# Performance work log

Hardware: AMD Instinct MI355X
Metric: run time of the kernel (lower is better)

The kernel has to match this reference:

```python
import jax, jax.numpy as jnp
import numpy as np

B, L, H, D = 2, 2048, 16, 64
E = H * D  # 1024

def setup_inputs() -> dict:
    key = jax.random.key(0)
    k1, k2, k3 = jax.random.split(key, 3)
    net_in = jax.random.normal(k1, (B, L, E), dtype=jnp.float32)
    # torch nn.Linear weights are [out_features, in_features]; scale like kaiming-uniform-ish
    W_qkv = jax.random.normal(k2, (3 * E, E), dtype=jnp.float32) * (1.0 / np.sqrt(E))
    W_out = jax.random.normal(k3, (E, E), dtype=jnp.float32) * (1.0 / np.sqrt(E))
    return {"net_in": net_in, "W_qkv": W_qkv, "W_out": W_out}

def reference(net_in, W_qkv, W_out):
    b, l, c = net_in.shape
    h, d = H, D
    # c_proj: x @ W_qkv.T -> (B, L, 3E), split into q, k, v
    qkv = jnp.einsum('blc,ec->ble', net_in, W_qkv)
    q, k, v = jnp.split(qkv, 3, axis=-1)
    # reshape to (B, H, L, D)
    q = q.reshape(b, l, h, d).transpose(0, 2, 1, 3)
    k = k.reshape(b, l, h, d).transpose(0, 2, 1, 3)
    v = v.reshape(b, l, h, d).transpose(0, 2, 1, 3)
    scale = 1.0 / np.sqrt(d).astype(np.float32)
    attn = jnp.einsum('bhqd,bhkd->bhqk', q, k) * scale  # (B, H, L, L)
    causal = jnp.tril(jnp.ones((l, l), dtype=bool))
    attn = jnp.where(causal[None, None, :, :], attn, -jnp.inf)
    attn = jax.nn.softmax(attn, axis=-1)
    out = jnp.einsum('bhqk,bhkd->bhqd', attn, v)  # (B, H, L, D)
    out = out.transpose(0, 2, 1, 3).reshape(b, l, c)
    return jnp.einsum('blc,ec->ble', out, W_out)
```

## Files before the change

kernel.cpp:

```cpp
#include <hip/hip_runtime.h>
#include <hip/hip_bf16.h>

#define LOG2E 1.44269504088896340736f

typedef __attribute__((ext_vector_type(8))) short s16x8;
typedef __attribute__((ext_vector_type(4))) short s16x4;
typedef __attribute__((ext_vector_type(2))) unsigned int u32x2;
typedef __attribute__((ext_vector_type(4))) float f32x4;
typedef __attribute__((ext_vector_type(16))) float f32x16;

__device__ inline short f2bf(float f) {
  __hip_bfloat16 h = __float2bfloat16(f);
  union { __hip_bfloat16 h; short s; } u; u.h = h; return u.s;
}

__device__ inline unsigned cvtpk(float lo, float hi) {
  unsigned r;
  asm("v_cvt_pk_bf16_f32 %0, %1, %2" : "=v"(r) : "v"(lo), "v"(hi));
  return r;
}

__device__ inline void gl_lds16(const void* g, void* l) {
  __builtin_amdgcn_global_load_lds(
      (const __attribute__((address_space(1))) void*)g,
      (__attribute__((address_space(3))) void*)l, 16, 0, 0);
}

__global__ __launch_bounds__(256)
void cvt_all(const float* __restrict__ Wqkv, const float* __restrict__ Wout,
             const float* __restrict__ net,
             short* __restrict__ dWqkv, short* __restrict__ dWout,
             short* __restrict__ dnet) {
  int bid = blockIdx.x;
  const float* src; short* dst; int i;
  if (bid < 3072)      { src = Wqkv; dst = dWqkv; i = bid * 256 + threadIdx.x; }
  else if (bid < 4096) { src = Wout; dst = dWout; i = (bid - 3072) * 256 + threadIdx.x; }
  else                 { src = net;  dst = dnet;  i = (bid - 4096) * 256 + threadIdx.x; }
  f32x4 v = ((const f32x4*)src)[i];
  s16x4 o;
  o[0] = f2bf(v[0]); o[1] = f2bf(v[1]); o[2] = f2bf(v[2]); o[3] = f2bf(v[3]);
  ((s16x4*)dst)[i] = o;
}

template<int OUTF32, int VTRANS, int NSUB>
__global__ __launch_bounds__(256)
void gemm128(const short* __restrict__ A, int lda,
             const short* __restrict__ B, int ldb,
             void* __restrict__ Cp, int ldc, int K) {
  int id = (int)(blockIdx.x + (blockIdx.y << 5));
  int xcd = id & 7, slot = id >> 3;
  int m0 = (slot & 31) * 128;
  int n0 = (xcd * NSUB + (slot >> 5)) * 128;
  int t = threadIdx.x;
  int w = t >> 6, lane = t & 63;
  int l16 = lane & 15, quad = lane >> 4;
  int wm = w >> 1, wn = w & 1;

  __shared__ __align__(16) short As[2][128 * 32];
  __shared__ __align__(16) short Bs[2][128 * 32];

  int scell = ((t & 3) ^ ((t >> 3) & 3)) * 8;
  const short* bsrc = B + (size_t)(n0 + (t >> 2)) * ldb + scell;
  const short* asrc = A + (size_t)(m0 + (t >> 2)) * lda + scell;
  int rcell = (quad ^ ((l16 >> 1) & 3)) * 8;

  f32x4 acc[4][4];
#pragma unroll
  for (int i = 0; i < 4; ++i)
#pragma unroll
    for (int j = 0; j < 4; ++j) acc[i][j] = (f32x4){0.f, 0.f, 0.f, 0.f};

#pragma unroll
  for (int r = 0; r < 2; ++r) {
    gl_lds16(asrc + (size_t)r * 64 * lda, (char*)As + r * 4096 + w * 1024);
    gl_lds16(bsrc + (size_t)r * 64 * ldb, (char*)Bs + r * 4096 + w * 1024);
  }
  __syncthreads();

  int nks = K >> 5;
  for (int ks = 0; ks < nks; ++ks) {
    int cur = ks & 1;
    if (ks + 1 < nks) {
      int k0 = (ks + 1) * 32;
      int nb = cur ^ 1;
#pragma unroll
      for (int r = 0; r < 2; ++r) {
        gl_lds16(asrc + k0 + (size_t)r * 64 * lda, (char*)As + nb * 8192 + r * 4096 + w * 1024);
        gl_lds16(bsrc + k0 + (size_t)r * 64 * ldb, (char*)Bs + nb * 8192 + r * 4096 + w * 1024);
      }
    }

    s16x8 af[4], bf[4];
#pragma unroll
    for (int i = 0; i < 4; ++i) {
      af[i] = *(const s16x8*)(As[cur] + (wm * 64 + i * 16 + l16) * 32 + rcell);
      bf[i] = *(const s16x8*)(Bs[cur] + (wn * 64 + i * 16 + l16) * 32 + rcell);
    }
#pragma unroll
    for (int i = 0; i < 4; ++i)
#pragma unroll
      for (int j = 0; j < 4; ++j)
        acc[i][j] = __builtin_amdgcn_mfma_f32_16x16x32_bf16(af[i], bf[j], acc[i][j], 0, 0, 0);

    __syncthreads();
  }

  if (VTRANS && n0 >= 2048) {
    short* Cs = (short*)Cp;
#pragma unroll
    for (int i = 0; i < 4; ++i)
#pragma unroll
      for (int j = 0; j < 4; ++j) {
        int colg = n0 + wn * 64 + j * 16 + l16;
        int d = colg & 63;
        size_t dst = (size_t)(m0 + wm * 64 + d) * ldc + (colg - d) + i * 16 + quad * 4;
        s16x4 ob;
#pragma unroll
        for (int rr = 0; rr < 4; ++rr) ob[rr] = f2bf(acc[i][j][rr]);
        *(s16x4*)(Cs + dst) = ob;
      }
  } else {
#pragma unroll
    for (int i = 0; i < 4; ++i)
#pragma unroll
      for (int j = 0; j < 4; ++j)
#pragma unroll
        for (int rr = 0; rr < 4; ++rr) {
          size_t row = m0 + wm * 64 + i * 16 + quad * 4 + rr;
          size_t col = n0 + wn * 64 + j * 16 + l16;
          if (OUTF32) ((float*)Cp)[row * ldc + col] = acc[i][j][rr];
          else        ((short*)Cp)[row * ldc + col] = f2bf(acc[i][j][rr]);
        }
  }
}

__global__ __launch_bounds__(256)
void gemm64(const short* __restrict__ A, int lda,
            const short* __restrict__ B, int ldb,
            float* __restrict__ C, int ldc, int K) {
  int id = (int)(blockIdx.x + (blockIdx.y << 5));
  int xcd = id & 7, slot = id >> 3;
  int m0 = slot * 64;
  int n0 = xcd * 128;
  int t = threadIdx.x;
  int w = t >> 6, lane = t & 63;
  int l16 = lane & 15, quad = lane >> 4;
  int wm = w & 1, wn = w >> 1;

  __shared__ __align__(16) short As[2][64 * 32];
  __shared__ __align__(16) short Bs[2][128 * 32];

  int scell = ((t & 3) ^ ((t >> 3) & 3)) * 8;
  const short* asrc = A + (size_t)(m0 + (t >> 2)) * lda + scell;
  const short* bsrc = B + (size_t)(n0 + (t >> 2)) * ldb + scell;
  int rcell = (quad ^ ((l16 >> 1) & 3)) * 8;

  f32x4 acc[2][4];
#pragma unroll
  for (int i = 0; i < 2; ++i)
#pragma unroll
    for (int j = 0; j < 4; ++j) acc[i][j] = (f32x4){0.f, 0.f, 0.f, 0.f};

  gl_lds16(asrc, (char*)As + w * 1024);
#pragma unroll
  for (int r = 0; r < 2; ++r)
    gl_lds16(bsrc + (size_t)r * 64 * ldb, (char*)Bs + r * 4096 + w * 1024);
  __syncthreads();

  int nks = K >> 5;
  for (int ks = 0; ks < nks; ++ks) {
    int cur = ks & 1;
    if (ks + 1 < nks) {
      int k0 = (ks + 1) * 32;
      int nb = cur ^ 1;
      gl_lds16(asrc + k0, (char*)As + nb * 4096 + w * 1024);
#pragma unroll
      for (int r = 0; r < 2; ++r)
        gl_lds16(bsrc + k0 + (size_t)r * 64 * ldb, (char*)Bs + nb * 8192 + r * 4096 + w * 1024);
    }

    s16x8 af[2], bf[4];
#pragma unroll
    for (int i = 0; i < 2; ++i)
      af[i] = *(const s16x8*)(As[cur] + (wm * 32 + i * 16 + l16) * 32 + rcell);
#pragma unroll
    for (int j = 0; j < 4; ++j)
      bf[j] = *(const s16x8*)(Bs[cur] + (wn * 64 + j * 16 + l16) * 32 + rcell);
#pragma unroll
    for (int i = 0; i < 2; ++i)
#pragma unroll
      for (int j = 0; j < 4; ++j)
        acc[i][j] = __builtin_amdgcn_mfma_f32_16x16x32_bf16(af[i], bf[j], acc[i][j], 0, 0, 0);

    __syncthreads();
  }

#pragma unroll
  for (int i = 0; i < 2; ++i)
#pragma unroll
    for (int j = 0; j < 4; ++j)
#pragma unroll
      for (int rr = 0; rr < 4; ++rr) {
        size_t row = m0 + wm * 32 + i * 16 + quad * 4 + rr;
        size_t col = n0 + wn * 64 + j * 16 + l16;
        C[row * ldc + col] = acc[i][j][rr];
      }
}

__global__ __launch_bounds__(256, 4)
void attn(short* __restrict__ qkv) {
  const int L = 2048, E3 = 3072, EO = 1024;
  int id = (int)(blockIdx.x + (blockIdx.y << 5));
  int xcd = id & 7;
  int s = id >> 3;
  int bh = xcd * 4 + (s & 3);
  int u = s >> 2;
  int vv = u & 15;
  int qidx = (u & 16) ? (31 - vv) : vv;
  int b = bh >> 4, h = bh & 15;
  int q0 = qidx * 64;
  int t = threadIdx.x;
  int wave = t >> 6, lane = t & 63;
  int qh = wave >> 1, kh = wave & 1;
  int l31 = lane & 31, hsel = lane >> 5;
  int khi4 = hsel * 4;
  int key = (lane >> 1) & 3;
  const float SENT = -3.0e38f;
  const float SC = 0.125f * LOG2E;

  __shared__ __align__(16) short Ks[2][2][64][32];
  __shared__ __align__(16) short Vt[2][2][64][32];

  int rowbase = b * L;

  s16x8 qf[4];
  {
    const short* qp = qkv + (size_t)(rowbase + q0 + qh * 32 + l31) * E3 + h * 64 + hsel * 8;
#pragma unroll
    for (int e = 0; e < 4; ++e) {
      s16x8 raw = *(const s16x8*)(qp + e * 16);
#pragma unroll
      for (int j = 0; j < 8; ++j) {
        union { float f; int i; } u2; u2.i = ((int)(unsigned short)raw[j]) << 16;
        raw[j] = f2bf(u2.f * SC);
      }
      qf[e] = raw;
    }
  }

  int scell = ((lane & 3) ^ ((lane >> 3) & 3)) * 8;
  const short* ksrc = qkv + (size_t)(rowbase + wave * 16 + (lane >> 2)) * E3 + EO
                      + h * 64 + scell;
  const short* vsrc = qkv + (size_t)(rowbase + wave * 16 + (lane >> 2)) * E3 + 2 * EO
                      + h * 64 + scell;

  float l_acc = 0.f;
  f32x16 o0 = (f32x16){0.f,0.f,0.f,0.f,0.f,0.f,0.f,0.f,0.f,0.f,0.f,0.f,0.f,0.f,0.f,0.f};
  f32x16 o1 = o0;

  int nkb = qidx + 1;

  gl_lds16(ksrc,      (char*)Ks + wave * 1024);
  gl_lds16(ksrc + 32, (char*)Ks + 4096 + wave * 1024);
  gl_lds16(vsrc,      (char*)Vt + wave * 1024);
  gl_lds16(vsrc + 32, (char*)Vt + 4096 + wave * 1024);

  for (int kb = 0; kb < nkb; ++kb) {
    int cur = kb & 1;
    __syncthreads();
    if (kb + 1 < nkb) {
      size_t koff = (size_t)((kb + 1) * 64) * E3;
      int nb = cur ^ 1;
      gl_lds16(ksrc + koff,      (char*)Ks + nb * 8192 + wave * 1024);
      gl_lds16(ksrc + koff + 32, (char*)Ks + nb * 8192 + 4096 + wave * 1024);
      gl_lds16(vsrc + koff,      (char*)Vt + nb * 8192 + wave * 1024);
      gl_lds16(vsrc + koff + 32, (char*)Vt + nb * 8192 + 4096 + wave * 1024);
    }

    int rel = (q0 + qh * 32) - (kb * 64 + kh * 32);
    if (rel > -32) {
      int krow = kh * 32 + l31;
      s16x8 kf0 = *(const s16x8*)(&Ks[cur][0][krow][((0 + hsel) ^ key) * 8]);
      s16x8 kf1 = *(const s16x8*)(&Ks[cur][0][krow][((2 + hsel) ^ key) * 8]);
      s16x8 kf2 = *(const s16x8*)(&Ks[cur][1][krow][((0 + hsel) ^ key) * 8]);
      s16x8 kf3 = *(const s16x8*)(&Ks[cur][1][krow][((2 + hsel) ^ key) * 8]);
      s16x8 vf00 = *(const s16x8*)(&Vt[cur][kh][ 0 + l31][((0 + hsel) ^ key) * 8]);
      s16x8 vf01 = *(const s16x8*)(&Vt[cur][kh][32 + l31][((0 + hsel) ^ key) * 8]);
      s16x8 vf10 = *(const s16x8*)(&Vt[cur][kh][ 0 + l31][((2 + hsel) ^ key) * 8]);
      s16x8 vf11 = *(const s16x8*)(&Vt[cur][kh][32 + l31][((2 + hsel) ^ key) * 8]);

      f32x16 sf = (f32x16){0.f,0.f,0.f,0.f,0.f,0.f,0.f,0.f,0.f,0.f,0.f,0.f,0.f,0.f,0.f,0.f};
      sf = __builtin_amdgcn_mfma_f32_32x32x16_bf16(kf0, qf[0], sf, 0, 0, 0);
      sf = __builtin_amdgcn_mfma_f32_32x32x16_bf16(kf1, qf[1], sf, 0, 0, 0);
      sf = __builtin_amdgcn_mfma_f32_32x32x16_bf16(kf2, qf[2], sf, 0, 0, 0);
      sf = __builtin_amdgcn_mfma_f32_32x32x16_bf16(kf3, qf[3], sf, 0, 0, 0);

      if (rel < 31) {
        int thr = rel + l31 - khi4;
#pragma unroll
        for (int r = 0; r < 16; ++r) {
          const int base_k = (r & 3) + 8 * (r >> 2);
          if (base_k > thr) sf[r] = SENT;
        }
      }

      float pv[16];
#pragma unroll
      for (int r = 0; r < 16; ++r) {
        pv[r] = __builtin_amdgcn_exp2f(sf[r]);
        l_acc += pv[r];
      }

      unsigned A0 = cvtpk(pv[0],  pv[1]),  A1 = cvtpk(pv[2],  pv[3]);
      unsigned B0 = cvtpk(pv[4],  pv[5]),  B1 = cvtpk(pv[6],  pv[7]);
      unsigned C0 = cvtpk(pv[8],  pv[9]),  C1 = cvtpk(pv[10], pv[11]);
      unsigned D0 = cvtpk(pv[12], pv[13]), D1 = cvtpk(pv[14], pv[15]);
      u32x2 sw0 = __builtin_amdgcn_permlane32_swap(A0, B0, false, false);
      u32x2 sw1 = __builtin_amdgcn_permlane32_swap(A1, B1, false, false);
      u32x2 sw2 = __builtin_amdgcn_permlane32_swap(C0, D0, false, false);
      u32x2 sw3 = __builtin_amdgcn_permlane32_swap(C1, D1, false, false);
      union { s16x8 v; unsigned u[4]; } P0, P1;
      P0.u[0] = sw0[0]; P0.u[1] = sw1[0]; P0.u[2] = sw0[1]; P0.u[3] = sw1[1];
      P1.u[0] = sw2[0]; P1.u[1] = sw3[0]; P1.u[2] = sw2[1]; P1.u[3] = sw3[1];

      o0 = __builtin_amdgcn_mfma_f32_32x32x16_bf16(vf00, P0.v, o0, 0, 0, 0);
      o0 = __builtin_amdgcn_mfma_f32_32x32x16_bf16(vf10, P1.v, o0, 0, 0, 0);
      o1 = __builtin_amdgcn_mfma_f32_32x32x16_bf16(vf01, P0.v, o1, 0, 0, 0);
      o1 = __builtin_amdgcn_mfma_f32_32x32x16_bf16(vf11, P1.v, o1, 0, 0, 0);
    }
  }

  l_acc += __shfl_xor(l_acc, 32);
  __syncthreads();
  float* fs = (float*)&Ks[0][0][0][0];
  float* lb = (float*)&Vt[0][0][0][0];
  if (kh) {
#pragma unroll
    for (int r = 0; r < 16; ++r) {
      fs[qh * 2048 + r * 64 + lane] = o0[r];
      fs[qh * 2048 + (16 + r) * 64 + lane] = o1[r];
    }
    if (lane < 32) lb[qh * 32 + lane] = l_acc;
  }
  __syncthreads();
  if (!kh) {
    float inv = 1.f / (l_acc + lb[qh * 32 + l31]);
    size_t obase = (size_t)(rowbase + q0 + qh * 32 + l31) * E3 + h * 64;
    int fb = qh * 2048;
#pragma unroll
    for (int g = 0; g < 4; ++g) {
      s16x4 w0, w1;
#pragma unroll
      for (int rr = 0; rr < 4; ++rr) {
        int r = g * 4 + rr;
        w0[rr] = f2bf((o0[r] + fs[fb + r * 64 + lane]) * inv);
        w1[rr] = f2bf((o1[r] + fs[fb + (16 + r) * 64 + lane]) * inv);
      }
      *(s16x4*)(qkv + obase + g * 8 + khi4) = w0;
      *(s16x4*)(qkv + obase + 32 + g * 8 + khi4) = w1;
    }
  }
}

extern "C" void kernel_launch(void* const* d_in, const int* in_sizes, int n_in,
                              void* d_out, int out_size, void* d_ws, size_t ws_size,
                              hipStream_t stream) {
  const float* net_in = (const float*)d_in[0];
  const float* W_qkv  = (const float*)d_in[1];
  const float* W_out  = (const float*)d_in[2];

  short* Wqkvb = (short*)d_ws;
  short* Woutb = Wqkvb + (size_t)3072 * 1024;
  short* qkv   = Woutb + (size_t)1024 * 1024;
  short* netb  = (short*)d_out;

  cvt_all<<<8192, 256, 0, stream>>>(W_qkv, W_out, net_in, Wqkvb, Woutb, netb);

  gemm128<0, 1, 3><<<dim3(32, 24), 256, 0, stream>>>(netb, 1024, Wqkvb, 1024,
                                                     qkv, 3072, 1024);
  attn<<<dim3(32, 32), 256, 0, stream>>>(qkv);
  gemm64<<<dim3(32, 16), 256, 0, stream>>>(qkv, 3072, Woutb, 1024,
                                           (float*)d_out, 1024, 1024);
}
```

Before: 165.0 us.

## Replace QKV projection GEMM with 256x256 tile, 8-wave, deeply pipelined kernel

Swaps the 128x128, 4-wave QKV GEMM for a 256x256 tile kernel with 512 threads. It uses 64-wide K steps, a 128KB double-buffered LDS ring with XOR swizzle, and interleaves global-to-LDS loads with MFMA phases using explicit barriers, vmcnt waits and setprio. The larger tile raises arithmetic intensity and cuts redundant operand loads, and the interleaving hides memory latency. In exchange only 192 blocks launch, which is under one block per CU on 256 CUs, and the kernel hardcodes the problem dimensions.

```diff
diff --git a/kernel.cpp b/kernel.cpp
--- a/kernel.cpp
+++ b/kernel.cpp
@@ -42,94 +42,134 @@
   ((s16x4*)dst)[i] = o;
 }
 
-template<int OUTF32, int VTRANS, int NSUB>
-__global__ __launch_bounds__(256)
-void gemm128(const short* __restrict__ A, int lda,
-             const short* __restrict__ B, int ldb,
-             void* __restrict__ Cp, int ldc, int K) {
-  int id = (int)(blockIdx.x + (blockIdx.y << 5));
-  int xcd = id & 7, slot = id >> 3;
-  int m0 = (slot & 31) * 128;
-  int n0 = (xcd * NSUB + (slot >> 5)) * 128;
+__global__ __launch_bounds__(512, 1)
+void gemm256(const short* __restrict__ A, const short* __restrict__ B,
+             short* __restrict__ Cp) {
+  const int lda = 1024, ldb = 1024, ldc = 3072;
+  int m0 = blockIdx.x * 256, n0 = blockIdx.y * 256;
   int t = threadIdx.x;
-  int w = t >> 6, lane = t & 63;
+  int wid = t >> 6, lane = t & 63;
   int l16 = lane & 15, quad = lane >> 4;
-  int wm = w >> 1, wn = w & 1;
-
-  __shared__ __align__(16) short As[2][128 * 32];
-  __shared__ __align__(16) short Bs[2][128 * 32];
-
-  int scell = ((t & 3) ^ ((t >> 3) & 3)) * 8;
-  const short* bsrc = B + (size_t)(n0 + (t >> 2)) * ldb + scell;
-  const short* asrc = A + (size_t)(m0 + (t >> 2)) * lda + scell;
-  int rcell = (quad ^ ((l16 >> 1) & 3)) * 8;
-
-  f32x4 acc[4][4];
-#pragma unroll
-  for (int i = 0; i < 4; ++i)
+  int wr = wid >> 2, wc = wid & 3;
+  int l8 = lane >> 3;
+  int sw = ((lane & 7) ^ l8) * 8;
+  int k7 = l16 & 7;
+
+  __shared__ __align__(16) short L[65536];
+  char* Lc = (char*)L;
+
+  f32x4 acc[8][4];
+#pragma unroll
+  for (int i = 0; i < 8; ++i)
 #pragma unroll
     for (int j = 0; j < 4; ++j) acc[i][j] = (f32x4){0.f, 0.f, 0.f, 0.f};
 
-#pragma unroll
-  for (int r = 0; r < 2; ++r) {
-    gl_lds16(asrc + (size_t)r * 64 * lda, (char*)As + r * 4096 + w * 1024);
-    gl_lds16(bsrc + (size_t)r * 64 * ldb, (char*)Bs + r * 4096 + w * 1024);
-  }
-  __syncthreads();
-
-  int nks = K >> 5;
-  for (int ks = 0; ks < nks; ++ks) {
-    int cur = ks & 1;
-    if (ks + 1 < nks) {
-      int k0 = (ks + 1) * 32;
-      int nb = cur ^ 1;
-#pragma unroll
-      for (int r = 0; r < 2; ++r) {
-        gl_lds16(asrc + k0 + (size_t)r * 64 * lda, (char*)As + nb * 8192 + r * 4096 + w * 1024);
-        gl_lds16(bsrc + k0 + (size_t)r * 64 * ldb, (char*)Bs + nb * 8192 + r * 4096 + w * 1024);
-      }
-    }
-
-    s16x8 af[4], bf[4];
-#pragma unroll
-    for (int i = 0; i < 4; ++i) {
-      af[i] = *(const s16x8*)(As[cur] + (wm * 64 + i * 16 + l16) * 32 + rcell);
-      bf[i] = *(const s16x8*)(Bs[cur] + (wn * 64 + i * 16 + l16) * 32 + rcell);
-    }
-#pragma unroll
-    for (int i = 0; i < 4; ++i)
-#pragma unroll
-      for (int j = 0; j < 4; ++j)
-        acc[i][j] = __builtin_amdgcn_mfma_f32_16x16x32_bf16(af[i], bf[j], acc[i][j], 0, 0, 0);
-
-    __syncthreads();
-  }
-
-  if (VTRANS && n0 >= 2048) {
-    short* Cs = (short*)Cp;
-#pragma unroll
-    for (int i = 0; i < 4; ++i)
-#pragma unroll
-      for (int j = 0; j < 4; ++j) {
-        int colg = n0 + wn * 64 + j * 16 + l16;
-        int d = colg & 63;
-        size_t dst = (size_t)(m0 + wm * 64 + d) * ldc + (colg - d) + i * 16 + quad * 4;
+  const short* Ab = A + (size_t)(m0 + wid * 16 + l8) * lda + sw;
+  const short* Bb = B + (size_t)(n0 + wid * 16 + l8) * ldb + sw;
+
+  auto stA = [&](int buf, int half, int kt) {
+#pragma unroll
+    for (int r = 0; r < 2; ++r)
+      gl_lds16(Ab + (size_t)(half * 128 + r * 8) * lda + kt * 64,
+               Lc + buf * 65536 + half * 16384 + wid * 2048 + r * 1024);
+  };
+  auto stB = [&](int buf, int half, int kt) {
+#pragma unroll
+    for (int r = 0; r < 2; ++r)
+      gl_lds16(Bb + (size_t)(half * 128 + r * 8) * ldb + kt * 64,
+               Lc + buf * 65536 + (2 + half) * 16384 + wid * 2048 + r * 1024);
+  };
+
+  s16x8 bfr[4][2], afr[2][2];
+  auto rdB = [&](int buf) {
+#pragma unroll
+    for (int n = 0; n < 4; ++n)
+#pragma unroll
+      for (int kc = 0; kc < 2; ++kc)
+        bfr[n][kc] = *(const s16x8*)(L + buf * 32768 + (2 + (wc >> 1)) * 8192
+                       + ((wc & 1) * 64 + n * 16 + l16) * 64
+                       + (((kc * 4 + quad) ^ k7) * 8));
+  };
+  auto rdA = [&](int buf, int ms) {
+#pragma unroll
+    for (int mi = 0; mi < 2; ++mi)
+#pragma unroll
+      for (int kc = 0; kc < 2; ++kc)
+        afr[mi][kc] = *(const s16x8*)(L + buf * 32768 + wr * 8192
+                        + ((ms + mi) * 16 + l16) * 64
+                        + (((kc * 4 + quad) ^ k7) * 8));
+  };
+  auto mm = [&](int ms) {
+    __builtin_amdgcn_s_setprio(1);
+#pragma unroll
+    for (int mi = 0; mi < 2; ++mi)
+#pragma unroll
+      for (int n = 0; n < 4; ++n)
+#pragma unroll
+        for (int kc = 0; kc < 2; ++kc)
+          acc[ms + mi][n] = __builtin_amdgcn_mfma_f32_16x16x32_bf16(
+              afr[mi][kc], bfr[n][kc], acc[ms + mi][n], 0, 0, 0);
+    __builtin_amdgcn_s_setprio(0);
+  };
+#define BAR asm volatile("s_barrier" ::: "memory")
+
+  stA(0, 0, 0); stA(0, 1, 0); stB(0, 0, 0); stB(0, 1, 0);
+  stB(1, 0, 1); stB(1, 1, 1);
+  asm volatile("s_waitcnt vmcnt(4)" ::: "memory");
+  BAR;
+
+  for (int j = 0; j < 8; ++j) {
+    int t1 = 2 * j + 1;
+    bool more = (j < 7);
+    rdB(0); rdA(0, 0); stA(1, 0, t1);
+    BAR; mm(0); BAR;
+    rdA(0, 2); stA(1, 1, t1);
+    BAR; mm(2); BAR;
+    rdA(0, 4); if (more) stB(0, 0, t1 + 1);
+    BAR; mm(4); BAR;
+    rdA(0, 6); if (more) stB(0, 1, t1 + 1);
+    BAR; mm(6);
+    if (more) { asm volatile("s_waitcnt vmcnt(4)" ::: "memory"); }
+    else      { asm volatile("s_waitcnt vmcnt(0)" ::: "memory"); }
+    BAR;
+    rdB(1); rdA(1, 0); if (more) stA(0, 0, t1 + 1);
+    BAR; mm(0); BAR;
+    rdA(1, 2); if (more) stA(0, 1, t1 + 1);
+    BAR; mm(2); BAR;
+    rdA(1, 4); if (more) stB(1, 0, t1 + 2);
+    BAR; mm(4); BAR;
+    rdA(1, 6); if (more) stB(1, 1, t1 + 2);
+    BAR; mm(6);
+    if (more) { asm volatile("s_waitcnt vmcnt(4)" ::: "memory"); }
+    else      { asm volatile("s_waitcnt vmcnt(0)" ::: "memory"); }
+    BAR;
+  }
+#undef BAR
+
+  if (n0 >= 2048) {
+#pragma unroll
+    for (int ms = 0; ms < 8; ++ms)
+#pragma unroll
+      for (int n = 0; n < 4; ++n) {
+        int d = n * 16 + l16;
+        int chunk = m0 + wr * 128 + (ms >> 2) * 64;
+        int tokoff = (ms & 3) * 16 + quad * 4;
+        size_t dst = (size_t)(chunk + d) * ldc + (n0 + wc * 64) + tokoff;
         s16x4 ob;
 #pragma unroll
-        for (int rr = 0; rr < 4; ++rr) ob[rr] = f2bf(acc[i][j][rr]);
-        *(s16x4*)(Cs + dst) = ob;
+        for (int rr = 0; rr < 4; ++rr) ob[rr] = f2bf(acc[ms][n][rr]);
+        *(s16x4*)(Cp + dst) = ob;
       }
   } else {
 #pragma unroll
-    for (int i = 0; i < 4; ++i)
-#pragma unroll
-      for (int j = 0; j < 4; ++j)
+    for (int ms = 0; ms < 8; ++ms)
+#pragma unroll
+      for (int n = 0; n < 4; ++n)
 #pragma unroll
         for (int rr = 0; rr < 4; ++rr) {
-          size_t row = m0 + wm * 64 + i * 16 + quad * 4 + rr;
-          size_t col = n0 + wn * 64 + j * 16 + l16;
-          if (OUTF32) ((float*)Cp)[row * ldc + col] = acc[i][j][rr];
-          else        ((short*)Cp)[row * ldc + col] = f2bf(acc[i][j][rr]);
+          size_t row = m0 + wr * 128 + ms * 16 + quad * 4 + rr;
+          size_t col = n0 + wc * 64 + n * 16 + l16;
+          Cp[row * ldc + col] = f2bf(acc[ms][n][rr]);
         }
   }
 }
@@ -376,8 +416,7 @@
 
   cvt_all<<<8192, 256, 0, stream>>>(W_qkv, W_out, net_in, Wqkvb, Woutb, netb);
 
-  gemm128<0, 1, 3><<<dim3(32, 24), 256, 0, stream>>>(netb, 1024, Wqkvb, 1024,
-                                                     qkv, 3072, 1024);
+  gemm256<<<dim3(16, 12), 512, 0, stream>>>(netb, Wqkvb, qkv);
   attn<<<dim3(32, 32), 256, 0, stream>>>(qkv);
   gemm64<<<dim3(32, 16), 256, 0, stream>>>(qkv, 3072, Woutb, 1024,
                                            (float*)d_out, 1024, 1024);
```

Result: no change. 163.2 us (-1.1%).
